# Kernel optimization log

Measured on AMD Instinct MI355X. Metric: run time of the kernel, lower is better.

The kernel has to match this reference:

```python
import jax, jax.numpy as jnp
import numpy as np
from jax import lax

X_DIM, Z_DIM, H_DIM, G_DIM, I_DIM = 1, 16, 16, 8, 16
T_LEN, BATCH = 512, 2048


def _lin_params(key, fan_in, fan_out):
    k1, k2 = jax.random.split(key)
    bound = 1.0 / np.sqrt(fan_in)
    W = jax.random.uniform(k1, (fan_out, fan_in), jnp.float32, -bound, bound)
    b = jax.random.uniform(k2, (fan_out,), jnp.float32, -bound, bound)
    return W, b


def setup_inputs() -> dict:
    key = jax.random.key(0)
    ks = jax.random.split(key, 12)
    x = jax.random.normal(ks[0], (T_LEN, BATCH, X_DIM), jnp.float32)
    eps_z = jax.random.normal(ks[1], (T_LEN, BATCH, Z_DIM), jnp.float32)
    # LSTM (pytorch layout: gates i,f,g,o stacked)
    bnd = 1.0 / np.sqrt(H_DIM)
    lstm_Wih = jax.random.uniform(ks[2], (4 * H_DIM, X_DIM), jnp.float32, -bnd, bnd)
    lstm_Whh = jax.random.uniform(ks[3], (4 * H_DIM, H_DIM), jnp.float32, -bnd, bnd)
    lstm_bih = jax.random.uniform(ks[4], (4 * H_DIM,), jnp.float32, -bnd, bnd)
    lstm_bhh = jax.random.uniform(ks[5], (4 * H_DIM,), jnp.float32, -bnd, bnd)
    comb_W1, comb_b1 = _lin_params(ks[6], Z_DIM + H_DIM, I_DIM)
    comb_W2, comb_b2 = _lin_params(jax.random.fold_in(ks[6], 1), I_DIM, G_DIM)
    enc_W1, enc_b1 = _lin_params(ks[7], G_DIM, I_DIM)
    enc_W2, enc_b2 = _lin_params(jax.random.fold_in(ks[7], 1), I_DIM, 2 * Z_DIM)
    dec_W1, dec_b1 = _lin_params(ks[8], Z_DIM, I_DIM)
    dec_W2, dec_b2 = _lin_params(jax.random.fold_in(ks[8], 1), I_DIM, 2 * X_DIM)
    tr_W1, tr_b1 = _lin_params(ks[9], Z_DIM, I_DIM)
    tr_W2, tr_b2 = _lin_params(jax.random.fold_in(ks[9], 1), I_DIM, 2 * Z_DIM)
    return dict(x=x, eps_z=eps_z,
                lstm_Wih=lstm_Wih, lstm_Whh=lstm_Whh, lstm_bih=lstm_bih, lstm_bhh=lstm_bhh,
                comb_W1=comb_W1, comb_b1=comb_b1, comb_W2=comb_W2, comb_b2=comb_b2,
                enc_W1=enc_W1, enc_b1=enc_b1, enc_W2=enc_W2, enc_b2=enc_b2,
                dec_W1=dec_W1, dec_b1=dec_b1, dec_W2=dec_W2, dec_b2=dec_b2,
                tr_W1=tr_W1, tr_b1=tr_b1, tr_W2=tr_W2, tr_b2=tr_b2)


def _dkf_forward(x, eps_z, lstm_Wih, lstm_Whh, lstm_bih, lstm_bhh,
                 comb_W1, comb_b1, comb_W2, comb_b2,
                 enc_W1, enc_b1, enc_W2, enc_b2,
                 dec_W1, dec_b1, dec_W2, dec_b2,
                 tr_W1, tr_b1, tr_W2, tr_b2):
    T, B, _ = x.shape
    H = lstm_Whh.shape[1]
    Z = eps_z.shape[-1]

    # ---- backward LSTM: run over time-reversed x, then reverse outputs ----
    def lstm_step(carry, xt):
        h, c = carry
        gates = xt @ lstm_Wih.T + lstm_bih + h @ lstm_Whh.T + lstm_bhh  # (B, 4H)
        i, f, g, o = jnp.split(gates, 4, axis=-1)
        c = jax.nn.sigmoid(f) * c + jax.nn.sigmoid(i) * jnp.tanh(g)
        h = jax.nn.sigmoid(o) * jnp.tanh(c)
        return (h, c), h

    h0 = jnp.zeros((B, H), x.dtype)
    c0 = jnp.zeros((B, H), x.dtype)
    _, hs = lax.scan(lstm_step, (h0, c0), x[::-1])
    h_seq = hs[::-1]  # (T, B, H)

    # ---- DKF inference loop: combiner -> encoder -> reparam sample ----
    def dkf_step(z_prev, inp):
        h_t, eps_t = inp
        hz = jnp.concatenate([h_t, z_prev], axis=-1)                 # (B, H+Z)
        g = jnp.tanh(hz @ comb_W1.T + comb_b1) @ comb_W2.T + comb_b2  # (B, G)
        e = jnp.tanh(g @ enc_W1.T + enc_b1) @ enc_W2.T + enc_b2       # (B, 2Z)
        mu_z, logvar_z = e[:, :Z], e[:, Z:]
        z = mu_z + eps_t * jnp.exp(0.5 * logvar_z)
        return z, (z, mu_z, logvar_z, z_prev)

    z0 = jnp.zeros((B, Z), x.dtype)
    _, (z_seq, mu_z, logvar_z, z_prev_seq) = lax.scan(dkf_step, z0, (h_seq, eps_z))

    # ---- decoder p(x|z) over the whole sequence ----
    d = jnp.tanh(z_seq @ dec_W1.T + dec_b1) @ dec_W2.T + dec_b2  # (T, B, 2*X)
    Xd = d.shape[-1] // 2
    mu_x, logvar_x = d[..., :Xd], d[..., Xd:]

    # ---- latent transition prior p(z_t | z_{t-1}) ----
    tr = jnp.tanh(z_prev_seq @ tr_W1.T + tr_b1) @ tr_W2.T + tr_b2  # (T, B, 2Z)
    mu_tr, logvar_tr = tr[..., :Z], tr[..., Z:]

    # single packed output: (T, B, 2*X + 4*Z)
    return jnp.concatenate([mu_x, logvar_x, mu_z, logvar_z, mu_tr, logvar_tr], axis=-1)


def reference(x, eps_z, lstm_Wih, lstm_Whh, lstm_bih, lstm_bhh,
              comb_W1, comb_b1, comb_W2, comb_b2,
              enc_W1, enc_b1, enc_W2, enc_b2,
              dec_W1, dec_b1, dec_W2, dec_b2,
              tr_W1, tr_b1, tr_W2, tr_b2):
    return _dkf_forward(x, eps_z, lstm_Wih, lstm_Whh, lstm_bih, lstm_bhh,
                        comb_W1, comb_b1, comb_W2, comb_b2,
                        enc_W1, enc_b1, enc_W2, enc_b2,
                        dec_W1, dec_b1, dec_W2, dec_b2,
                        tr_W1, tr_b1, tr_W2, tr_b2)
```

## Files before the change

### kernel.cpp

```cpp
#include <hip/hip_runtime.h>

#define T_LEN 512
#define BATCH 2048
#define OUTW  66

typedef unsigned int u32;
typedef short v8s __attribute__((ext_vector_type(8)));
typedef float v4f __attribute__((ext_vector_type(4)));
typedef float v2f __attribute__((ext_vector_type(2)));
typedef u32   v2u __attribute__((ext_vector_type(2)));

union FragU { v8s s; u32 w[4]; };

__device__ __forceinline__ float fexp2(float x){ return __builtin_amdgcn_exp2f(x); }
__device__ __forceinline__ float frcp (float x){ return __builtin_amdgcn_rcpf(x); }
__device__ __forceinline__ float ftanh(float x){
    return fmaf(2.f, frcp(1.f + fexp2(-2.88539008f * x)), -1.f);
}
__device__ __forceinline__ float fsig(float x){
    return frcp(1.f + fexp2(-1.44269504f * x));
}
__device__ __forceinline__ u32 cvtpk(float lo, float hi){
    u32 r; asm("v_cvt_pk_bf16_f32 %0, %1, %2" : "=v"(r) : "v"(lo), "v"(hi)); return r;
}
__device__ __forceinline__ float ubf_lo(u32 w){ union{u32 i; float f;} v; v.i = w << 16;         return v.f; }
__device__ __forceinline__ float ubf_hi(u32 w){ union{u32 i; float f;} v; v.i = w & 0xffff0000u; return v.f; }
__device__ __forceinline__ u32 bperm(int addr, u32 v){ return (u32)__builtin_amdgcn_ds_bpermute(addr, (int)v); }
__device__ __forceinline__ void packpair(float a, float b, u32& wh, u32& wl){
    u32 h = cvtpk(a, b);
    wl = cvtpk(a - ubf_lo(h), b - ubf_hi(h));
    wh = h;
}
#define MFMA(A,B,C) __builtin_amdgcn_mfma_f32_16x16x32_bf16((A),(B),(C),0,0,0)

__device__ __forceinline__ void loadAsplit(const float* W, int ld, int R, int C,
                                           v8s& hi, v8s& lo){
    const int r = threadIdx.x & 15, G = threadIdx.x >> 4;
    FragU H, L;
#pragma unroll
    for (int p = 0; p < 4; ++p){
        const int k0 = 8*G + 2*p;
        float a = (r < R && k0     < C) ? W[r*ld + k0]     : 0.f;
        float b = (r < R && k0 + 1 < C) ? W[r*ld + k0 + 1] : 0.f;
        packpair(a, b, H.w[p], L.w[p]);
    }
    hi = H.s; lo = L.s;
}
__device__ __forceinline__ v8s loadA1(const float* W, int ld, int R, int C){
    const int r = threadIdx.x & 15, G = threadIdx.x >> 4;
    FragU H;
#pragma unroll
    for (int p = 0; p < 4; ++p){
        const int k0 = 8*G + 2*p;
        float a = (r < R && k0     < C) ? W[r*ld + k0]     : 0.f;
        float b = (r < R && k0 + 1 < C) ? W[r*ld + k0 + 1] : 0.f;
        H.w[p] = cvtpk(a, b);
    }
    return H.s;
}
__device__ __forceinline__ v4f loadCbias(const float* bsrc, int R){
    const int m = threadIdx.x >> 4;
    v4f c;
#pragma unroll
    for (int j = 0; j < 4; ++j){
        const int idx = 4*m + j;
        c[j] = (idx < R) ? bsrc[idx] : 0.f;
    }
    return c;
}
__device__ __forceinline__ void splitB(v4f d, int alo, int ahi, bool uz,
                                       v8s& bh, v8s& bl){
    u32 h0, l0, h1, l1;
    packpair(d[0], d[1], h0, l0);
    packpair(d[2], d[3], h1, l1);
    FragU H, L;
    H.w[0] = bperm(alo, h0); H.w[1] = bperm(alo, h1);
    H.w[2] = bperm(ahi, h0); H.w[3] = bperm(ahi, h1);
    L.w[0] = bperm(alo, l0); L.w[1] = bperm(alo, l1);
    L.w[2] = bperm(ahi, l0); L.w[3] = bperm(ahi, l1);
    if (uz){
#pragma unroll
        for (int p = 0; p < 4; ++p){ H.w[p] = 0u; L.w[p] = 0u; }
    }
    bh = H.s; bl = L.s;
}
__device__ __forceinline__ v4f tanh4(v4f a){
    v4f r;
#pragma unroll
    for (int j = 0; j < 4; ++j) r[j] = ftanh(a[j]);
    return r;
}
__device__ __forceinline__ void st2(float* p, float a, float b){
    v2f v; v[0] = a; v[1] = b; *(v2f*)p = v;
}
__device__ __forceinline__ void loadHfrag(const float* out, int t, int bc, int G,
                                          v8s& hh, v8s& hl){
    if (G < 2){
        const float* o = out + (size_t)(t*BATCH + bc) * OUTW;
        v2u a0 = *(const v2u*)(o + 34 + 4*G);
        v2u a1 = *(const v2u*)(o + 36 + 4*G);
        v2u b0 = *(const v2u*)(o + 42 + 4*G);
        v2u b1 = *(const v2u*)(o + 44 + 4*G);
        FragU H, L;
        H.w[0]=a0[0]; H.w[1]=a0[1]; H.w[2]=a1[0]; H.w[3]=a1[1];
        L.w[0]=b0[0]; L.w[1]=b0[1]; L.w[2]=b1[0]; L.w[3]=b1[1];
        hh = H.s; hl = L.s;
    } else {
        FragU Z; Z.w[0]=Z.w[1]=Z.w[2]=Z.w[3]=0u;
        hh = Z.s; hl = Z.s;
    }
}

__global__ __launch_bounds__(64)
void dkf_mfma_kernel(const float* __restrict__ x,   const float* __restrict__ eps_z,
                     const float* __restrict__ Wih, const float* __restrict__ Whh,
                     const float* __restrict__ bih, const float* __restrict__ bhh,
                     const float* __restrict__ cW1, const float* __restrict__ cb1,
                     const float* __restrict__ cW2, const float* __restrict__ cb2,
                     const float* __restrict__ eW1, const float* __restrict__ eb1,
                     const float* __restrict__ eW2, const float* __restrict__ eb2,
                     const float* __restrict__ dW1, const float* __restrict__ db1,
                     const float* __restrict__ dW2, const float* __restrict__ db2,
                     const float* __restrict__ tW1, const float* __restrict__ tb1,
                     const float* __restrict__ tW2, const float* __restrict__ tb2,
                     float* __restrict__ out)
{
    const int lane = threadIdx.x;
    const int c    = lane & 15;
    const int G    = lane >> 4;
    const int b0   = blockIdx.x * 16;
    const int bc   = b0 + c;
    const bool uz  = (G >= 2);
    const int alo  = 4 * (32*G + c);
    const int ahi  = alo + 64;

    {
        v8s whT_h[4], whT_l[4];
#pragma unroll
        for (int g = 0; g < 4; ++g)
            loadAsplit(Whh + 256*g, 16, 16, 16, whT_h[g], whT_l[g]);
        v4f bc4[4];
#pragma unroll
        for (int g = 0; g < 4; ++g){
            v4f t;
#pragma unroll
            for (int j = 0; j < 4; ++j){
                const int idx = 16*g + 4*G + j;
                t[j] = bih[idx] + bhh[idx];
            }
            bc4[g] = t;
        }
        float wihr[4][4];
#pragma unroll
        for (int g = 0; g < 4; ++g)
#pragma unroll
            for (int j = 0; j < 4; ++j) wihr[g][j] = Wih[16*g + 4*G + j];

        v4f cst = {0.f, 0.f, 0.f, 0.f};
        FragU Z0; Z0.w[0]=Z0.w[1]=Z0.w[2]=Z0.w[3]=0u;
        v8s hhi = Z0.s, hlo = Z0.s;
        float xv[2];
        xv[0] = x[(T_LEN-1)*BATCH + bc];
        xv[1] = x[(T_LEN-2)*BATCH + bc];

        for (int t2 = 0; t2 < T_LEN/2; ++t2){
#pragma unroll
            for (int q = 0; q < 2; ++q){
                const int t = T_LEN - 1 - 2*t2 - q;
                v4f di = MFMA(whT_h[0], hhi, bc4[0]); di = MFMA(whT_h[0], hlo, di); di = MFMA(whT_l[0], hhi, di);
                v4f df = MFMA(whT_h[1], hhi, bc4[1]); df = MFMA(whT_h[1], hlo, df); df = MFMA(whT_l[1], hhi, df);
                v4f dg = MFMA(whT_h[2], hhi, bc4[2]); dg = MFMA(whT_h[2], hlo, dg); dg = MFMA(whT_l[2], hhi, dg);
                v4f doo= MFMA(whT_h[3], hhi, bc4[3]); doo= MFMA(whT_h[3], hlo, doo); doo= MFMA(whT_l[3], hhi, doo);
#pragma unroll
                for (int j = 0; j < 4; ++j){
                    di[j]  = fmaf(wihr[0][j], xv[q], di[j]);
                    df[j]  = fmaf(wihr[1][j], xv[q], df[j]);
                    dg[j]  = fmaf(wihr[2][j], xv[q], dg[j]);
                    doo[j] = fmaf(wihr[3][j], xv[q], doo[j]);
                }
                v4f hv;
#pragma unroll
                for (int j = 0; j < 4; ++j){
                    const float si = fsig(di[j]);
                    const float sf = fsig(df[j]);
                    const float tg = ftanh(dg[j]);
                    const float so = fsig(doo[j]);
                    cst[j] = fmaf(sf, cst[j], si * tg);
                    hv[j]  = so * ftanh(cst[j]);
                }
                u32 h0, l0, h1, l1;
                packpair(hv[0], hv[1], h0, l0);
                packpair(hv[2], hv[3], h1, l1);
                {
                    float* o = out + (size_t)(t*BATCH + bc) * OUTW;
                    v2u sh; sh[0] = h0; sh[1] = h1;
                    v2u sl; sl[0] = l0; sl[1] = l1;
                    *(v2u*)(o + 34 + 2*G) = sh;
                    *(v2u*)(o + 42 + 2*G) = sl;
                }
                FragU H, L;
                H.w[0] = bperm(alo, h0); H.w[1] = bperm(alo, h1);
                H.w[2] = bperm(ahi, h0); H.w[3] = bperm(ahi, h1);
                L.w[0] = bperm(alo, l0); L.w[1] = bperm(alo, l1);
                L.w[2] = bperm(ahi, l0); L.w[3] = bperm(ahi, l1);
                if (uz){
#pragma unroll
                    for (int p = 0; p < 4; ++p){ H.w[p] = 0u; L.w[p] = 0u; }
                }
                hhi = H.s; hlo = L.s;
                const int tn = (t >= 2) ? (t - 2) : 0;
                xv[q] = x[tn*BATCH + bc];
            }
        }
    }

    __threadfence();

    v8s aC1h_h, aC1h_l; loadAsplit(cW1,       32, 16, 16, aC1h_h, aC1h_l);
    v8s aC1z_h, aC1z_l; loadAsplit(cW1 + 16,  32, 16, 16, aC1z_h, aC1z_l);
    v8s aC2_h,  aC2_l;  loadAsplit(cW2,       16,  8, 16, aC2_h,  aC2_l);
    v8s aE1_h,  aE1_l;  loadAsplit(eW1,        8, 16,  8, aE1_h,  aE1_l);
    v8s aE2m_h, aE2m_l; loadAsplit(eW2,       16, 16, 16, aE2m_h, aE2m_l);
    v8s aE2v_h, aE2v_l; loadAsplit(eW2 + 256, 16, 16, 16, aE2v_h, aE2v_l);
    v8s aD1  = loadA1(dW1,       16, 16, 16);
    v8s aD2  = loadA1(dW2,       16,  2, 16);
    v8s aT1  = loadA1(tW1,       16, 16, 16);
    v8s aT2m = loadA1(tW2,       16, 16, 16);
    v8s aT2v = loadA1(tW2 + 256, 16, 16, 16);
    const v4f bC1  = loadCbias(cb1, 16);
    const v4f bC2  = loadCbias(cb2,  8);
    const v4f bE1  = loadCbias(eb1, 16);
    const v4f bE2m = loadCbias(eb2, 16);
    const v4f bE2v = loadCbias(eb2 + 16, 16);
    const v4f bD1  = loadCbias(db1, 16);
    const v4f bD2  = loadCbias(db2,  2);
    const v4f bT1  = loadCbias(tb1, 16);
    const v4f bT2m = loadCbias(tb2, 16);
    const v4f bT2v = loadCbias(tb2 + 16, 16);

    FragU Z1; Z1.w[0]=Z1.w[1]=Z1.w[2]=Z1.w[3]=0u;
    v8s zh = Z1.s, zl = Z1.s;

    v8s hhr[2], hlr[2];
    v4f epr[2];
    loadHfrag(out, 0, bc, G, hhr[0], hlr[0]);
    loadHfrag(out, 1, bc, G, hhr[1], hlr[1]);
    epr[0] = *(const v4f*)(eps_z + (size_t)(0*BATCH + bc)*16 + 4*G);
    epr[1] = *(const v4f*)(eps_z + (size_t)(1*BATCH + bc)*16 + 4*G);

    for (int t2 = 0; t2 < T_LEN/2; ++t2){
#pragma unroll
        for (int q = 0; q < 2; ++q){
            const int t = 2*t2 + q;
            float* o = out + (size_t)(t*BATCH + bc) * OUTW;
            const v8s hh = hhr[q], hl = hlr[q];
            const v4f ep = epr[q];
            {
                int tn = t + 2; if (tn >= T_LEN) tn = T_LEN - 1;
                loadHfrag(out, tn, bc, G, hhr[q], hlr[q]);
                epr[q] = *(const v4f*)(eps_z + (size_t)(tn*BATCH + bc)*16 + 4*G);
            }
            v4f dt1 = MFMA(aT1, zh, bT1); dt1 = MFMA(aT1, zl, dt1);
            v4f at  = tanh4(dt1);
            v8s ath, atl; splitB(at, alo, ahi, uz, ath, atl);
            v4f dmt = MFMA(aT2m, ath, bT2m); dmt = MFMA(aT2m, atl, dmt);
            v4f dlt = MFMA(aT2v, ath, bT2v); dlt = MFMA(aT2v, atl, dlt);
            v4f d1 = MFMA(aC1h_h, hh, bC1);
            d1 = MFMA(aC1h_h, hl, d1);
            d1 = MFMA(aC1h_l, hh, d1);
            d1 = MFMA(aC1z_h, zh, d1);
            d1 = MFMA(aC1z_h, zl, d1);
            d1 = MFMA(aC1z_l, zh, d1);
            v4f a1 = tanh4(d1);
            v8s a1h, a1l; splitB(a1, alo, ahi, uz, a1h, a1l);
            v4f d2 = MFMA(aC2_h, a1h, bC2); d2 = MFMA(aC2_h, a1l, d2); d2 = MFMA(aC2_l, a1h, d2);
            v8s gh, gl; splitB(d2, alo, ahi, uz, gh, gl);
            v4f d3 = MFMA(aE1_h, gh, bE1); d3 = MFMA(aE1_h, gl, d3); d3 = MFMA(aE1_l, gh, d3);
            v4f e1 = tanh4(d3);
            v8s e1h, e1l; splitB(e1, alo, ahi, uz, e1h, e1l);
            v4f dmu = MFMA(aE2m_h, e1h, bE2m); dmu = MFMA(aE2m_h, e1l, dmu); dmu = MFMA(aE2m_l, e1h, dmu);
            v4f dlv = MFMA(aE2v_h, e1h, bE2v); dlv = MFMA(aE2v_h, e1l, dlv); dlv = MFMA(aE2v_l, e1h, dlv);
            v4f zv;
#pragma unroll
            for (int j = 0; j < 4; ++j){
                const float s = fexp2(0.72134752f * fminf(dlv[j], 40.f));
                zv[j] = fmaf(ep[j], s, dmu[j]);
            }
            splitB(zv, alo, ahi, uz, zh, zl);
            v4f dd1 = MFMA(aD1, zh, bD1); dd1 = MFMA(aD1, zl, dd1);
            v4f ad  = tanh4(dd1);
            v8s adh, adl; splitB(ad, alo, ahi, uz, adh, adl);
            v4f dd2 = MFMA(aD2, adh, bD2); dd2 = MFMA(aD2, adl, dd2);
            st2(o +  2 + 4*G, dmu[0], dmu[1]); st2(o +  4 + 4*G, dmu[2], dmu[3]);
            st2(o + 18 + 4*G, dlv[0], dlv[1]); st2(o + 20 + 4*G, dlv[2], dlv[3]);
            st2(o + 34 + 4*G, dmt[0], dmt[1]); st2(o + 36 + 4*G, dmt[2], dmt[3]);
            st2(o + 50 + 4*G, dlt[0], dlt[1]); st2(o + 52 + 4*G, dlt[2], dlt[3]);
            if (lane < 16) st2(o, dd2[0], dd2[1]);
        }
    }
}

extern "C" void kernel_launch(void* const* d_in, const int* in_sizes, int n_in,
                              void* d_out, int out_size, void* d_ws, size_t ws_size,
                              hipStream_t stream) {
    (void)in_sizes; (void)n_in; (void)out_size; (void)d_ws; (void)ws_size;
    const float* x     = (const float*)d_in[0];
    const float* eps_z = (const float*)d_in[1];
    const float* Wih   = (const float*)d_in[2];
    const float* Whh   = (const float*)d_in[3];
    const float* bih   = (const float*)d_in[4];
    const float* bhh   = (const float*)d_in[5];
    const float* cW1   = (const float*)d_in[6];
    const float* cb1   = (const float*)d_in[7];
    const float* cW2   = (const float*)d_in[8];
    const float* cb2   = (const float*)d_in[9];
    const float* eW1   = (const float*)d_in[10];
    const float* eb1   = (const float*)d_in[11];
    const float* eW2   = (const float*)d_in[12];
    const float* eb2   = (const float*)d_in[13];
    const float* dW1   = (const float*)d_in[14];
    const float* db1   = (const float*)d_in[15];
    const float* dW2   = (const float*)d_in[16];
    const float* db2   = (const float*)d_in[17];
    const float* tW1   = (const float*)d_in[18];
    const float* tb1   = (const float*)d_in[19];
    const float* tW2   = (const float*)d_in[20];
    const float* tb2   = (const float*)d_in[21];

    dkf_mfma_kernel<<<BATCH/16, 64, 0, stream>>>(
        x, eps_z, Wih, Whh, bih, bhh,
        cW1, cb1, cW2, cb2, eW1, eb1, eW2, eb2,
        dW1, db1, dW2, db2, tW1, tb1, tW2, tb2,
        (float*)d_out);
}
```

Measured before the change: 1.140 ms.

## Pack hi/lo bf16 splits into one K=32 fragment via permlane swaps

Replaces the ds_bpermute-based B-fragment redistribution with v_permlane32/16 swaps, and packs the hi and lo bf16 halves of each 16-wide activation into the unused upper K half of the 16x16x32 MFMA. Each split-precision product now needs two MFMAs instead of three, and single-precision ones need one instead of two. This shortens the serial recurrent chain in both the LSTM and DKF loops and removes the LDS-path permutes. The A-fragment layout duplicates the weights across K halves so that the hi*lo cross terms are preserved.

```diff
diff --git a/kernel.cpp b/kernel.cpp
--- a/kernel.cpp
+++ b/kernel.cpp
@@ -25,35 +25,56 @@
 }
 __device__ __forceinline__ float ubf_lo(u32 w){ union{u32 i; float f;} v; v.i = w << 16;         return v.f; }
 __device__ __forceinline__ float ubf_hi(u32 w){ union{u32 i; float f;} v; v.i = w & 0xffff0000u; return v.f; }
-__device__ __forceinline__ u32 bperm(int addr, u32 v){ return (u32)__builtin_amdgcn_ds_bpermute(addr, (int)v); }
-__device__ __forceinline__ void packpair(float a, float b, u32& wh, u32& wl){
-    u32 h = cvtpk(a, b);
-    wl = cvtpk(a - ubf_lo(h), b - ubf_hi(h));
-    wh = h;
+__device__ __forceinline__ void pswap32(u32& a, u32& b){
+    asm("v_permlane32_swap_b32 %0, %1" : "+v"(a), "+v"(b));
+}
+__device__ __forceinline__ void pswap16(u32& a, u32& b){
+    asm("v_permlane16_swap_b32 %0, %1" : "+v"(a), "+v"(b));
 }
 #define MFMA(A,B,C) __builtin_amdgcn_mfma_f32_16x16x32_bf16((A),(B),(C),0,0,0)
 
+__device__ __forceinline__ void pack4(v4f d, u32& Ah, u32& Bh, u32& Al, u32& Bl){
+    Ah = cvtpk(d[0], d[1]);
+    Bh = cvtpk(d[2], d[3]);
+    Al = cvtpk(d[0] - ubf_lo(Ah), d[1] - ubf_hi(Ah));
+    Bl = cvtpk(d[2] - ubf_lo(Bh), d[3] - ubf_hi(Bh));
+}
+__device__ __forceinline__ v8s swizB(u32 Ah, u32 Bh, u32 Al, u32 Bl){
+    pswap32(Ah, Al); pswap16(Ah, Al);
+    pswap32(Bh, Bl); pswap16(Bh, Bl);
+    FragU F; F.w[0] = Ah; F.w[1] = Bh; F.w[2] = Al; F.w[3] = Bl;
+    return F.s;
+}
+__device__ __forceinline__ v8s reB(v4f d){
+    u32 Ah, Bh, Al, Bl; pack4(d, Ah, Bh, Al, Bl);
+    return swizB(Ah, Bh, Al, Bl);
+}
 __device__ __forceinline__ void loadAsplit(const float* W, int ld, int R, int C,
-                                           v8s& hi, v8s& lo){
+                                           v8s& A1, v8s& A2){
     const int r = threadIdx.x & 15, G = threadIdx.x >> 4;
+    const int g2 = G & 1;
     FragU H, L;
 #pragma unroll
     for (int p = 0; p < 4; ++p){
-        const int k0 = 8*G + 2*p;
-        float a = (r < R && k0     < C) ? W[r*ld + k0]     : 0.f;
-        float b = (r < R && k0 + 1 < C) ? W[r*ld + k0 + 1] : 0.f;
-        packpair(a, b, H.w[p], L.w[p]);
-    }
-    hi = H.s; lo = L.s;
+        const int k0 = 8*g2 + 2*p;
+        const float a = (r < R && k0     < C) ? W[r*ld + k0]     : 0.f;
+        const float b = (r < R && k0 + 1 < C) ? W[r*ld + k0 + 1] : 0.f;
+        const u32 h = cvtpk(a, b);
+        const u32 l = cvtpk(a - ubf_lo(h), b - ubf_hi(h));
+        H.w[p] = h;
+        L.w[p] = (G < 2) ? l : 0u;
+    }
+    A1 = H.s; A2 = L.s;
 }
 __device__ __forceinline__ v8s loadA1(const float* W, int ld, int R, int C){
     const int r = threadIdx.x & 15, G = threadIdx.x >> 4;
+    const int g2 = G & 1;
     FragU H;
 #pragma unroll
     for (int p = 0; p < 4; ++p){
-        const int k0 = 8*G + 2*p;
-        float a = (r < R && k0     < C) ? W[r*ld + k0]     : 0.f;
-        float b = (r < R && k0 + 1 < C) ? W[r*ld + k0 + 1] : 0.f;
+        const int k0 = 8*g2 + 2*p;
+        const float a = (r < R && k0     < C) ? W[r*ld + k0]     : 0.f;
+        const float b = (r < R && k0 + 1 < C) ? W[r*ld + k0 + 1] : 0.f;
         H.w[p] = cvtpk(a, b);
     }
     return H.s;
@@ -68,22 +89,6 @@
     }
     return c;
 }
-__device__ __forceinline__ void splitB(v4f d, int alo, int ahi, bool uz,
-                                       v8s& bh, v8s& bl){
-    u32 h0, l0, h1, l1;
-    packpair(d[0], d[1], h0, l0);
-    packpair(d[2], d[3], h1, l1);
-    FragU H, L;
-    H.w[0] = bperm(alo, h0); H.w[1] = bperm(alo, h1);
-    H.w[2] = bperm(ahi, h0); H.w[3] = bperm(ahi, h1);
-    L.w[0] = bperm(alo, l0); L.w[1] = bperm(alo, l1);
-    L.w[2] = bperm(ahi, l0); L.w[3] = bperm(ahi, l1);
-    if (uz){
-#pragma unroll
-        for (int p = 0; p < 4; ++p){ H.w[p] = 0u; L.w[p] = 0u; }
-    }
-    bh = H.s; bl = L.s;
-}
 __device__ __forceinline__ v4f tanh4(v4f a){
     v4f r;
 #pragma unroll
@@ -93,22 +98,13 @@
 __device__ __forceinline__ void st2(float* p, float a, float b){
     v2f v; v[0] = a; v[1] = b; *(v2f*)p = v;
 }
-__device__ __forceinline__ void loadHfrag(const float* out, int t, int bc, int G,
-                                          v8s& hh, v8s& hl){
-    if (G < 2){
-        const float* o = out + (size_t)(t*BATCH + bc) * OUTW;
-        v2u a0 = *(const v2u*)(o + 34 + 4*G);
-        v2u a1 = *(const v2u*)(o + 36 + 4*G);
-        v2u b0 = *(const v2u*)(o + 42 + 4*G);
-        v2u b1 = *(const v2u*)(o + 44 + 4*G);
-        FragU H, L;
-        H.w[0]=a0[0]; H.w[1]=a0[1]; H.w[2]=a1[0]; H.w[3]=a1[1];
-        L.w[0]=b0[0]; L.w[1]=b0[1]; L.w[2]=b1[0]; L.w[3]=b1[1];
-        hh = H.s; hl = L.s;
-    } else {
-        FragU Z; Z.w[0]=Z.w[1]=Z.w[2]=Z.w[3]=0u;
-        hh = Z.s; hl = Z.s;
-    }
+__device__ __forceinline__ v8s loadHfrag(const float* out, int t, int bc, int G){
+    const float* o = out + (size_t)(t*BATCH + bc) * OUTW;
+    FragU F;
+    v2u a = *(const v2u*)(o + 34 + 4*G);
+    v2u b = *(const v2u*)(o + 36 + 4*G);
+    F.w[0] = a[0]; F.w[1] = a[1]; F.w[2] = b[0]; F.w[3] = b[1];
+    return F.s;
 }
 
 __global__ __launch_bounds__(64)
@@ -128,17 +124,13 @@
     const int lane = threadIdx.x;
     const int c    = lane & 15;
     const int G    = lane >> 4;
-    const int b0   = blockIdx.x * 16;
-    const int bc   = b0 + c;
-    const bool uz  = (G >= 2);
-    const int alo  = 4 * (32*G + c);
-    const int ahi  = alo + 64;
+    const int bc   = blockIdx.x * 16 + c;
 
     {
-        v8s whT_h[4], whT_l[4];
+        v8s A1g[4], A2g[4];
 #pragma unroll
         for (int g = 0; g < 4; ++g)
-            loadAsplit(Whh + 256*g, 16, 16, 16, whT_h[g], whT_l[g]);
+            loadAsplit(Whh + 256*g, 16, 16, 16, A1g[g], A2g[g]);
         v4f bc4[4];
 #pragma unroll
         for (int g = 0; g < 4; ++g){
@@ -158,7 +150,7 @@
 
         v4f cst = {0.f, 0.f, 0.f, 0.f};
         FragU Z0; Z0.w[0]=Z0.w[1]=Z0.w[2]=Z0.w[3]=0u;
-        v8s hhi = Z0.s, hlo = Z0.s;
+        v8s hb = Z0.s;
         float xv[2];
         xv[0] = x[(T_LEN-1)*BATCH + bc];
         xv[1] = x[(T_LEN-2)*BATCH + bc];
@@ -167,17 +159,18 @@
 #pragma unroll
             for (int q = 0; q < 2; ++q){
                 const int t = T_LEN - 1 - 2*t2 - q;
-                v4f di = MFMA(whT_h[0], hhi, bc4[0]); di = MFMA(whT_h[0], hlo, di); di = MFMA(whT_l[0], hhi, di);
-                v4f df = MFMA(whT_h[1], hhi, bc4[1]); df = MFMA(whT_h[1], hlo, df); df = MFMA(whT_l[1], hhi, df);
-                v4f dg = MFMA(whT_h[2], hhi, bc4[2]); dg = MFMA(whT_h[2], hlo, dg); dg = MFMA(whT_l[2], hhi, dg);
-                v4f doo= MFMA(whT_h[3], hhi, bc4[3]); doo= MFMA(whT_h[3], hlo, doo); doo= MFMA(whT_l[3], hhi, doo);
+                v4f ci, cf, cg, co;
 #pragma unroll
                 for (int j = 0; j < 4; ++j){
-                    di[j]  = fmaf(wihr[0][j], xv[q], di[j]);
-                    df[j]  = fmaf(wihr[1][j], xv[q], df[j]);
-                    dg[j]  = fmaf(wihr[2][j], xv[q], dg[j]);
-                    doo[j] = fmaf(wihr[3][j], xv[q], doo[j]);
+                    ci[j] = fmaf(wihr[0][j], xv[q], bc4[0][j]);
+                    cf[j] = fmaf(wihr[1][j], xv[q], bc4[1][j]);
+                    cg[j] = fmaf(wihr[2][j], xv[q], bc4[2][j]);
+                    co[j] = fmaf(wihr[3][j], xv[q], bc4[3][j]);
                 }
+                v4f di  = MFMA(A1g[0], hb, ci); di  = MFMA(A2g[0], hb, di);
+                v4f df  = MFMA(A1g[1], hb, cf); df  = MFMA(A2g[1], hb, df);
+                v4f dg  = MFMA(A1g[2], hb, cg); dg  = MFMA(A2g[2], hb, dg);
+                v4f doo = MFMA(A1g[3], hb, co); doo = MFMA(A2g[3], hb, doo);
                 v4f hv;
 #pragma unroll
                 for (int j = 0; j < 4; ++j){
@@ -188,26 +181,16 @@
                     cst[j] = fmaf(sf, cst[j], si * tg);
                     hv[j]  = so * ftanh(cst[j]);
                 }
-                u32 h0, l0, h1, l1;
-                packpair(hv[0], hv[1], h0, l0);
-                packpair(hv[2], hv[3], h1, l1);
+                u32 Ah, Bh, Al, Bl;
+                pack4(hv, Ah, Bh, Al, Bl);
                 {
                     float* o = out + (size_t)(t*BATCH + bc) * OUTW;
-                    v2u sh; sh[0] = h0; sh[1] = h1;
-                    v2u sl; sl[0] = l0; sl[1] = l1;
+                    v2u sh; sh[0] = Ah; sh[1] = Bh;
+                    v2u sl; sl[0] = Al; sl[1] = Bl;
                     *(v2u*)(o + 34 + 2*G) = sh;
                     *(v2u*)(o + 42 + 2*G) = sl;
                 }
-                FragU H, L;
-                H.w[0] = bperm(alo, h0); H.w[1] = bperm(alo, h1);
-                H.w[2] = bperm(ahi, h0); H.w[3] = bperm(ahi, h1);
-                L.w[0] = bperm(alo, l0); L.w[1] = bperm(alo, l1);
-                L.w[2] = bperm(ahi, l0); L.w[3] = bperm(ahi, l1);
-                if (uz){
-#pragma unroll
-                    for (int p = 0; p < 4; ++p){ H.w[p] = 0u; L.w[p] = 0u; }
-                }
-                hhi = H.s; hlo = L.s;
+                hb = swizB(Ah, Bh, Al, Bl);
                 const int tn = (t >= 2) ? (t - 2) : 0;
                 xv[q] = x[tn*BATCH + bc];
             }
@@ -216,17 +199,17 @@
 
     __threadfence();
 
-    v8s aC1h_h, aC1h_l; loadAsplit(cW1,       32, 16, 16, aC1h_h, aC1h_l);
-    v8s aC1z_h, aC1z_l; loadAsplit(cW1 + 16,  32, 16, 16, aC1z_h, aC1z_l);
-    v8s aC2_h,  aC2_l;  loadAsplit(cW2,       16,  8, 16, aC2_h,  aC2_l);
-    v8s aE1_h,  aE1_l;  loadAsplit(eW1,        8, 16,  8, aE1_h,  aE1_l);
-    v8s aE2m_h, aE2m_l; loadAsplit(eW2,       16, 16, 16, aE2m_h, aE2m_l);
-    v8s aE2v_h, aE2v_l; loadAsplit(eW2 + 256, 16, 16, 16, aE2v_h, aE2v_l);
-    v8s aD1  = loadA1(dW1,       16, 16, 16);
-    v8s aD2  = loadA1(dW2,       16,  2, 16);
-    v8s aT1  = loadA1(tW1,       16, 16, 16);
-    v8s aT2m = loadA1(tW2,       16, 16, 16);
-    v8s aT2v = loadA1(tW2 + 256, 16, 16, 16);
+    v8s C1h1, C1h2; loadAsplit(cW1,       32, 16, 16, C1h1, C1h2);
+    v8s C1z1, C1z2; loadAsplit(cW1 + 16,  32, 16, 16, C1z1, C1z2);
+    v8s C21,  C22;  loadAsplit(cW2,       16,  8, 16, C21,  C22);
+    v8s E11,  E12;  loadAsplit(eW1,        8, 16,  8, E11,  E12);
+    v8s E2m1, E2m2; loadAsplit(eW2,       16, 16, 16, E2m1, E2m2);
+    v8s E2v1, E2v2; loadAsplit(eW2 + 256, 16, 16, 16, E2v1, E2v2);
+    v8s D1  = loadA1(dW1,       16, 16, 16);
+    v8s D2  = loadA1(dW2,       16,  2, 16);
+    v8s T1  = loadA1(tW1,       16, 16, 16);
+    v8s T2m = loadA1(tW2,       16, 16, 16);
+    v8s T2v = loadA1(tW2 + 256, 16, 16, 16);
     const v4f bC1  = loadCbias(cb1, 16);
     const v4f bC2  = loadCbias(cb2,  8);
     const v4f bE1  = loadCbias(eb1, 16);
@@ -239,12 +222,12 @@
     const v4f bT2v = loadCbias(tb2 + 16, 16);
 
     FragU Z1; Z1.w[0]=Z1.w[1]=Z1.w[2]=Z1.w[3]=0u;
-    v8s zh = Z1.s, zl = Z1.s;
-
-    v8s hhr[2], hlr[2];
+    v8s zb = Z1.s;
+
+    v8s hbr[2];
     v4f epr[2];
-    loadHfrag(out, 0, bc, G, hhr[0], hlr[0]);
-    loadHfrag(out, 1, bc, G, hhr[1], hlr[1]);
+    hbr[0] = loadHfrag(out, 0, bc, G);
+    hbr[1] = loadHfrag(out, 1, bc, G);
     epr[0] = *(const v4f*)(eps_z + (size_t)(0*BATCH + bc)*16 + 4*G);
     epr[1] = *(const v4f*)(eps_z + (size_t)(1*BATCH + bc)*16 + 4*G);
 
@@ -253,44 +236,42 @@
         for (int q = 0; q < 2; ++q){
             const int t = 2*t2 + q;
             float* o = out + (size_t)(t*BATCH + bc) * OUTW;
-            const v8s hh = hhr[q], hl = hlr[q];
+            const v8s hb = hbr[q];
             const v4f ep = epr[q];
             {
                 int tn = t + 2; if (tn >= T_LEN) tn = T_LEN - 1;
-                loadHfrag(out, tn, bc, G, hhr[q], hlr[q]);
+                hbr[q] = loadHfrag(out, tn, bc, G);
                 epr[q] = *(const v4f*)(eps_z + (size_t)(tn*BATCH + bc)*16 + 4*G);
             }
-            v4f dt1 = MFMA(aT1, zh, bT1); dt1 = MFMA(aT1, zl, dt1);
+            v4f dt1 = MFMA(T1, zb, bT1);
             v4f at  = tanh4(dt1);
-            v8s ath, atl; splitB(at, alo, ahi, uz, ath, atl);
-            v4f dmt = MFMA(aT2m, ath, bT2m); dmt = MFMA(aT2m, atl, dmt);
-            v4f dlt = MFMA(aT2v, ath, bT2v); dlt = MFMA(aT2v, atl, dlt);
-            v4f d1 = MFMA(aC1h_h, hh, bC1);
-            d1 = MFMA(aC1h_h, hl, d1);
-            d1 = MFMA(aC1h_l, hh, d1);
-            d1 = MFMA(aC1z_h, zh, d1);
-            d1 = MFMA(aC1z_h, zl, d1);
-            d1 = MFMA(aC1z_l, zh, d1);
-            v4f a1 = tanh4(d1);
-            v8s a1h, a1l; splitB(a1, alo, ahi, uz, a1h, a1l);
-            v4f d2 = MFMA(aC2_h, a1h, bC2); d2 = MFMA(aC2_h, a1l, d2); d2 = MFMA(aC2_l, a1h, d2);
-            v8s gh, gl; splitB(d2, alo, ahi, uz, gh, gl);
-            v4f d3 = MFMA(aE1_h, gh, bE1); d3 = MFMA(aE1_h, gl, d3); d3 = MFMA(aE1_l, gh, d3);
-            v4f e1 = tanh4(d3);
-            v8s e1h, e1l; splitB(e1, alo, ahi, uz, e1h, e1l);
-            v4f dmu = MFMA(aE2m_h, e1h, bE2m); dmu = MFMA(aE2m_h, e1l, dmu); dmu = MFMA(aE2m_l, e1h, dmu);
-            v4f dlv = MFMA(aE2v_h, e1h, bE2v); dlv = MFMA(aE2v_h, e1l, dlv); dlv = MFMA(aE2v_l, e1h, dlv);
+            v8s atb = reB(at);
+            v4f dmt = MFMA(T2m, atb, bT2m);
+            v4f dlt = MFMA(T2v, atb, bT2v);
+            v4f d1 = MFMA(C1h1, hb, bC1);
+            d1 = MFMA(C1h2, hb, d1);
+            d1 = MFMA(C1z1, zb, d1);
+            d1 = MFMA(C1z2, zb, d1);
+            v4f a1  = tanh4(d1);
+            v8s a1b = reB(a1);
+            v4f d2 = MFMA(C21, a1b, bC2); d2 = MFMA(C22, a1b, d2);
+            v8s gb2 = reB(d2);
+            v4f d3 = MFMA(E11, gb2, bE1); d3 = MFMA(E12, gb2, d3);
+            v4f e1  = tanh4(d3);
+            v8s e1b = reB(e1);
+            v4f dmu = MFMA(E2m1, e1b, bE2m); dmu = MFMA(E2m2, e1b, dmu);
+            v4f dlv = MFMA(E2v1, e1b, bE2v); dlv = MFMA(E2v2, e1b, dlv);
             v4f zv;
 #pragma unroll
             for (int j = 0; j < 4; ++j){
                 const float s = fexp2(0.72134752f * fminf(dlv[j], 40.f));
                 zv[j] = fmaf(ep[j], s, dmu[j]);
             }
-            splitB(zv, alo, ahi, uz, zh, zl);
-            v4f dd1 = MFMA(aD1, zh, bD1); dd1 = MFMA(aD1, zl, dd1);
+            zb = reB(zv);
+            v4f dd1 = MFMA(D1, zb, bD1);
             v4f ad  = tanh4(dd1);
-            v8s adh, adl; splitB(ad, alo, ahi, uz, adh, adl);
-            v4f dd2 = MFMA(aD2, adh, bD2); dd2 = MFMA(aD2, adl, dd2);
+            v8s adb = reB(ad);
+            v4f dd2 = MFMA(D2, adb, bD2);
             st2(o +  2 + 4*G, dmu[0], dmu[1]); st2(o +  4 + 4*G, dmu[2], dmu[3]);
             st2(o + 18 + 4*G, dlv[0], dlv[1]); st2(o + 20 + 4*G, dlv[2], dlv[3]);
             st2(o + 34 + 4*G, dmt[0], dmt[1]); st2(o + 36 + 4*G, dmt[2], dmt[3]);
```

Result: faster. 1.004 ms (-12.0%).
